# Kernel optimization log

Measured on AMD Instinct MI355X. Metric: run time of the kernel, lower is better.

Reference implementation:

```python
import jax, jax.numpy as jnp
import numpy as np

B, N, C = 4, 2048, 1024
H = 16
HD = C // H  # head_dim = 64


def setup_inputs() -> dict:
    key = jax.random.key(0)
    k1, k2, k3 = jax.random.split(key, 3)
    x = jax.random.normal(k1, (B, N, C), dtype=jnp.float32)
    # nn.Linear-style init scale ~ 1/sqrt(fan_in)
    W_qkv = jax.random.normal(k2, (3 * C, C), dtype=jnp.float32) / np.sqrt(C)
    W_proj = jax.random.normal(k3, (C, C), dtype=jnp.float32) / np.sqrt(C)
    b_proj = jnp.zeros((C,), dtype=jnp.float32)
    return {"x": x, "W_qkv": W_qkv, "W_proj": W_proj, "b_proj": b_proj}


def reference(x, W_qkv, W_proj, b_proj):
    Bb, Nn, Cc = x.shape
    scale = (Cc // H) ** -0.5
    # qkv: [B,N,3C] -> [3,B,H,N,HD]
    qkv = jnp.einsum('bnc,dc->bnd', x, W_qkv)
    qkv = qkv.reshape(Bb, Nn, 3, H, Cc // H).transpose(2, 0, 3, 1, 4)
    q, k, v = qkv[0] * scale, qkv[1], qkv[2]
    attn = jnp.einsum('bhqd,bhkd->bhqk', q, k)  # [B,H,N,N]
    attn = jax.nn.softmax(attn, axis=-1)
    out = jnp.einsum('bhqk,bhkd->bhqd', attn, v)  # [B,H,N,HD]
    out = out.transpose(0, 2, 1, 3).reshape(Bb, Nn, Cc)
    return jnp.einsum('bnc,dc->bnd', out, W_proj) + b_proj
```

## Files before the change

kernel.cpp:

```cpp
#include <hip/hip_runtime.h>

typedef _Float16 f16;
typedef _Float16 half8 __attribute__((ext_vector_type(8)));
typedef _Float16 half4 __attribute__((ext_vector_type(4)));
typedef __fp16 fp16x2 __attribute__((ext_vector_type(2)));
typedef float float4_ __attribute__((ext_vector_type(4)));
typedef float f32x16 __attribute__((ext_vector_type(16)));
typedef unsigned int uint2_ __attribute__((ext_vector_type(2)));

#define MFMA16(a, b, c) __builtin_amdgcn_mfma_f32_16x16x32_f16(a, b, c, 0, 0, 0)
#define MFMA32(a, b, c) __builtin_amdgcn_mfma_f32_32x32x16_f16(a, b, c, 0, 0, 0)

__device__ __forceinline__ void gld_lds16(const void* g, void* l) {
    __builtin_amdgcn_global_load_lds(
        (const __attribute__((address_space(1))) void*)g,
        (__attribute__((address_space(3))) void*)l, 16, 0, 0);
}

__device__ __forceinline__ unsigned pkrtz(float a, float b) {
    union { fp16x2 h; unsigned u; } c;
    c.h = __builtin_amdgcn_cvt_pkrtz(a, b);
    return c.u;
}

__device__ __forceinline__ float max3f(float a, float b, float c) {
    float d;
    asm("v_max3_f32 %0, %1, %2, %3" : "=v"(d) : "v"(a), "v"(b), "v"(c));
    return d;
}

__global__ void cast_kernel(const float* __restrict__ in, f16* __restrict__ out,
                            int n, int qboundary, float qscale) {
    int i = (blockIdx.x * blockDim.x + threadIdx.x) * 4;
    if (i >= n) return;
    float4_ v = *(const float4_*)(in + i);
    float sc = (i < qboundary) ? qscale : 1.0f;
    half4 h;
    h[0] = (f16)(v[0] * sc);
    h[1] = (f16)(v[1] * sc);
    h[2] = (f16)(v[2] * sc);
    h[3] = (f16)(v[3] * sc);
    *(half4*)(out + i) = h;
}

__global__ __launch_bounds__(256, 2)
void qkv_gemm(const f16* __restrict__ X, const f16* __restrict__ W,
              f16* __restrict__ Q, f16* __restrict__ Kq, f16* __restrict__ V) {
    const int K = 1024;
    __shared__ __align__(16) f16 sA[128 * 64];
    __shared__ __align__(16) f16 sB[128 * 64];
    int tid = threadIdx.x;
    int lane = tid & 63, wave = tid >> 6;
    int wm = wave >> 1, wn = wave & 1;
    int l15 = lane & 15, quad = lane >> 4;
    int rowBase = blockIdx.y * 128;
    int colBase = blockIdx.x * 128;

    float4_ acc[4][4] = {};

    for (int k0 = 0; k0 < K; k0 += 64) {
        for (int i = 0; i < 4; ++i) {
            int seg = wave * 4 + i;
            int e = (seg * 64 + lane) * 8;
            int r = e >> 6, c = e & 63;
            gld_lds16(X + (size_t)(rowBase + r) * K + k0 + c, sA + seg * 512);
            gld_lds16(W + (size_t)(colBase + r) * K + k0 + c, sB + seg * 512);
        }
        __syncthreads();
        for (int ks = 0; ks < 2; ++ks) {
            half8 a[4], b[4];
            for (int mt = 0; mt < 4; ++mt)
                a[mt] = *(const half8*)&sA[(wm * 64 + mt * 16 + l15) * 64 + ks * 32 + quad * 8];
            for (int nt = 0; nt < 4; ++nt)
                b[nt] = *(const half8*)&sB[(wn * 64 + nt * 16 + l15) * 64 + ks * 32 + quad * 8];
            for (int mt = 0; mt < 4; ++mt)
                for (int nt = 0; nt < 4; ++nt)
                    acc[mt][nt] = MFMA16(a[mt], b[nt], acc[mt][nt]);
        }
        __syncthreads();
    }

    for (int mt = 0; mt < 4; ++mt) {
        int m0 = rowBase + wm * 64 + mt * 16 + quad * 4;
        for (int nt = 0; nt < 4; ++nt) {
            int d = colBase + wn * 64 + nt * 16 + l15;
            int part = d >> 10;
            int h = (d >> 6) & 15;
            int hd = d & 63;
            f16* dst = (part == 0) ? Q : (part == 1) ? Kq : V;
            for (int r = 0; r < 4; ++r) {
                int m = m0 + r;
                int b = m >> 11, n = m & 2047;
                dst[(size_t)((b * 16 + h) * 2048 + n) * 64 + hd] = (f16)acc[mt][nt][r];
            }
        }
    }
}

__global__ __launch_bounds__(256, 2)
void attn_kernel(const f16* __restrict__ Q, const f16* __restrict__ Kk,
                 const f16* __restrict__ V, f16* __restrict__ O) {
    int L = blockIdx.y * gridDim.x + blockIdx.x;
    int m_ = L & 63;
    int bh = (m_ & 7) * 8 + (m_ >> 3);
    int qt = L >> 6;
    const f16* Qb = Q + (size_t)bh * 2048 * 64;
    const f16* Kb = Kk + (size_t)bh * 2048 * 64;
    const f16* Vb = V + (size_t)bh * 2048 * 64;
    int tid = threadIdx.x, lane = tid & 63, wave = tid >> 6;
    int l31 = lane & 31, hi = lane >> 5;

    __shared__ __align__(16) f16 Vt[2][64 * 72];

    int qbase = qt * 128 + wave * 32;

    half8 aQ[4];
#pragma unroll
    for (int d = 0; d < 4; ++d)
        aQ[d] = *(const half8*)(Qb + (size_t)(qbase + l31) * 64 + d * 16 + hi * 8);

    f32x16 oacc0 = {}, oacc1 = {}, lacc = {};
    float mrow = -1e30f;

    half8 vone;
#pragma unroll
    for (int j = 0; j < 8; ++j) vone[j] = (f16)1.0f;

    half8 bK0[4], bK1[4];
#pragma unroll
    for (int d = 0; d < 4; ++d) {
        bK0[d] = *(const half8*)(Kb + (size_t)(l31) * 64 + d * 16 + hi * 8);
        bK1[d] = *(const half8*)(Kb + (size_t)(32 + l31) * 64 + d * 16 + hi * 8);
    }
    {
        const f16* vsrc = Vb + (size_t)lane * 64 + wave * 16;
        half8 v0 = *(const half8*)(vsrc);
        half8 v1 = *(const half8*)(vsrc + 8);
#pragma unroll
        for (int j = 0; j < 8; ++j) {
            Vt[0][(wave * 16 + j) * 72 + lane] = v0[j];
            Vt[0][(wave * 16 + 8 + j) * 72 + lane] = v1[j];
        }
    }

#pragma unroll 2
    for (int it = 0; it < 32; ++it) {
        int buf = it & 1;
        __syncthreads();

        f32x16 s0 = {}, s1 = {};
        __builtin_amdgcn_s_setprio(1);
#pragma unroll
        for (int d = 0; d < 4; ++d) s0 = MFMA32(bK0[d], aQ[d], s0);
#pragma unroll
        for (int d = 0; d < 4; ++d) s1 = MFMA32(bK1[d], aQ[d], s1);
        __builtin_amdgcn_s_setprio(0);

        half8 bK0n[4], bK1n[4], v0n, v1n;
        if (it < 31) {
            int t1 = (it + 1) * 64;
#pragma unroll
            for (int d = 0; d < 4; ++d) {
                bK0n[d] = *(const half8*)(Kb + (size_t)(t1 + l31) * 64 + d * 16 + hi * 8);
                bK1n[d] = *(const half8*)(Kb + (size_t)(t1 + 32 + l31) * 64 + d * 16 + hi * 8);
            }
            const f16* vsrc = Vb + (size_t)(t1 + lane) * 64 + wave * 16;
            v0n = *(const half8*)(vsrc);
            v1n = *(const half8*)(vsrc + 8);
        }

        float a0 = max3f(s0[0], s0[1], s0[2]);
        float a1 = max3f(s0[3], s0[4], s0[5]);
        float a2 = max3f(s0[6], s0[7], s0[8]);
        float a3 = max3f(s0[9], s0[10], s0[11]);
        float a4 = max3f(s0[12], s0[13], s0[14]);
        float a5 = max3f(s0[15], s1[0], s1[1]);
        float a6 = max3f(s1[2], s1[3], s1[4]);
        float a7 = max3f(s1[5], s1[6], s1[7]);
        float a8 = max3f(s1[8], s1[9], s1[10]);
        float a9 = max3f(s1[11], s1[12], s1[13]);
        float a10 = fmaxf(s1[14], s1[15]);
        float b0 = max3f(a0, a1, a2);
        float b1 = max3f(a3, a4, a5);
        float b2 = max3f(a6, a7, a8);
        float b3 = fmaxf(a9, a10);
        float mx = fmaxf(max3f(b0, b1, b2), b3);
        mx = fmaxf(mx, __shfl_xor(mx, 32, 64));

        if (__any(mx > mrow + 8.0f)) {
            float mnew = fmaxf(mrow, mx);
            float alpha = exp2f(mrow - mnew);
            mrow = mnew;
#pragma unroll
            for (int r = 0; r < 16; ++r) {
                int cr = (r & 3) + 8 * (r >> 2) + 4 * hi;
                float ar = __shfl(alpha, cr, 64);
                oacc0[r] *= ar;
                oacc1[r] *= ar;
                lacc[r] *= ar;
            }
        }

#pragma unroll
        for (int r = 0; r < 16; ++r) s0[r] = exp2f(s0[r] - mrow);
#pragma unroll
        for (int r = 0; r < 16; ++r) s1[r] = exp2f(s1[r] - mrow);

        half8 PA[4];
        {
            union { half8 h; unsigned u[4]; } w;
            uint2_ r02 = __builtin_amdgcn_permlane32_swap(pkrtz(s0[0], s0[1]), pkrtz(s0[4], s0[5]), false, false);
            uint2_ r13 = __builtin_amdgcn_permlane32_swap(pkrtz(s0[2], s0[3]), pkrtz(s0[6], s0[7]), false, false);
            w.u[0] = r02[0]; w.u[1] = r13[0]; w.u[2] = r02[1]; w.u[3] = r13[1];
            PA[0] = w.h;
            r02 = __builtin_amdgcn_permlane32_swap(pkrtz(s0[8], s0[9]), pkrtz(s0[12], s0[13]), false, false);
            r13 = __builtin_amdgcn_permlane32_swap(pkrtz(s0[10], s0[11]), pkrtz(s0[14], s0[15]), false, false);
            w.u[0] = r02[0]; w.u[1] = r13[0]; w.u[2] = r02[1]; w.u[3] = r13[1];
            PA[1] = w.h;
            r02 = __builtin_amdgcn_permlane32_swap(pkrtz(s1[0], s1[1]), pkrtz(s1[4], s1[5]), false, false);
            r13 = __builtin_amdgcn_permlane32_swap(pkrtz(s1[2], s1[3]), pkrtz(s1[6], s1[7]), false, false);
            w.u[0] = r02[0]; w.u[1] = r13[0]; w.u[2] = r02[1]; w.u[3] = r13[1];
            PA[2] = w.h;
            r02 = __builtin_amdgcn_permlane32_swap(pkrtz(s1[8], s1[9]), pkrtz(s1[12], s1[13]), false, false);
            r13 = __builtin_amdgcn_permlane32_swap(pkrtz(s1[10], s1[11]), pkrtz(s1[14], s1[15]), false, false);
            w.u[0] = r02[0]; w.u[1] = r13[0]; w.u[2] = r02[1]; w.u[3] = r13[1];
            PA[3] = w.h;
        }

        __builtin_amdgcn_s_setprio(1);
#pragma unroll
        for (int ks = 0; ks < 4; ++ks) {
            half8 vf0 = *(const half8*)&Vt[buf][(l31) * 72 + ks * 16 + hi * 8];
            half8 vf1 = *(const half8*)&Vt[buf][(32 + l31) * 72 + ks * 16 + hi * 8];
            oacc0 = MFMA32(PA[ks], vf0, oacc0);
            oacc1 = MFMA32(PA[ks], vf1, oacc1);
            lacc = MFMA32(PA[ks], vone, lacc);
        }
        __builtin_amdgcn_s_setprio(0);

        if (it < 31) {
#pragma unroll
            for (int j = 0; j < 8; ++j) {
                Vt[buf ^ 1][(wave * 16 + j) * 72 + lane] = v0n[j];
                Vt[buf ^ 1][(wave * 16 + 8 + j) * 72 + lane] = v1n[j];
            }
#pragma unroll
            for (int d = 0; d < 4; ++d) {
                bK0[d] = bK0n[d];
                bK1[d] = bK1n[d];
            }
        }
    }

    int b = bh >> 4, h = bh & 15;
#pragma unroll
    for (int r = 0; r < 16; ++r) {
        int cr = (r & 3) + 8 * (r >> 2) + 4 * hi;
        int n = qbase + cr;
        float inv = 1.0f / lacc[r];
        O[(size_t)(b * 2048 + n) * 1024 + h * 64 + l31] = (f16)(oacc0[r] * inv);
        O[(size_t)(b * 2048 + n) * 1024 + h * 64 + 32 + l31] = (f16)(oacc1[r] * inv);
    }
}

__global__ __launch_bounds__(256, 2)
void proj_gemm(const f16* __restrict__ A, const f16* __restrict__ W,
               const float* __restrict__ bias, float* __restrict__ out) {
    const int K = 1024;
    __shared__ __align__(16) f16 sA[128 * 64];
    __shared__ __align__(16) f16 sB[128 * 64];
    int tid = threadIdx.x;
    int lane = tid & 63, wave = tid >> 6;
    int wm = wave >> 1, wn = wave & 1;
    int l15 = lane & 15, quad = lane >> 4;
    int rowBase = blockIdx.y * 128;
    int colBase = blockIdx.x * 128;

    float4_ acc[4][4] = {};

    for (int k0 = 0; k0 < K; k0 += 64) {
        for (int i = 0; i < 4; ++i) {
            int seg = wave * 4 + i;
            int e = (seg * 64 + lane) * 8;
            int r = e >> 6, c = e & 63;
            gld_lds16(A + (size_t)(rowBase + r) * K + k0 + c, sA + seg * 512);
            gld_lds16(W + (size_t)(colBase + r) * K + k0 + c, sB + seg * 512);
        }
        __syncthreads();
        for (int ks = 0; ks < 2; ++ks) {
            half8 a[4], b[4];
            for (int mt = 0; mt < 4; ++mt)
                a[mt] = *(const half8*)&sA[(wm * 64 + mt * 16 + l15) * 64 + ks * 32 + quad * 8];
            for (int nt = 0; nt < 4; ++nt)
                b[nt] = *(const half8*)&sB[(wn * 64 + nt * 16 + l15) * 64 + ks * 32 + quad * 8];
            for (int mt = 0; mt < 4; ++mt)
                for (int nt = 0; nt < 4; ++nt)
                    acc[mt][nt] = MFMA16(a[mt], b[nt], acc[mt][nt]);
        }
        __syncthreads();
    }

    for (int mt = 0; mt < 4; ++mt) {
        int m0 = rowBase + wm * 64 + mt * 16 + quad * 4;
        for (int nt = 0; nt < 4; ++nt) {
            int d = colBase + wn * 64 + nt * 16 + l15;
            float bv = bias[d];
            for (int r = 0; r < 4; ++r) {
                int m = m0 + r;
                out[(size_t)m * 1024 + d] = acc[mt][nt][r] + bv;
            }
        }
    }
}

extern "C" void kernel_launch(void* const* d_in, const int* in_sizes, int n_in,
                              void* d_out, int out_size, void* d_ws, size_t ws_size,
                              hipStream_t stream) {
    const float* x     = (const float*)d_in[0];
    const float* Wqkv  = (const float*)d_in[1];
    const float* Wproj = (const float*)d_in[2];
    const float* bproj = (const float*)d_in[3];
    float* out = (float*)d_out;

    f16* ws     = (f16*)d_ws;
    f16* xb     = ws;
    f16* wqkvb  = xb + 8388608;
    f16* wprojb = wqkvb + 3145728;
    f16* q      = wprojb + 1048576;
    f16* k      = q + 8388608;
    f16* v      = k + 8388608;
    f16* ao     = v + 8388608;

    const float qscale = 0.125f * 1.4426950408889634f;

    cast_kernel<<<8192, 256, 0, stream>>>(x, xb, 8388608, 0, 1.f);
    cast_kernel<<<3072, 256, 0, stream>>>(Wqkv, wqkvb, 3145728, 1048576, qscale);
    cast_kernel<<<1024, 256, 0, stream>>>(Wproj, wprojb, 1048576, 0, 1.f);

    qkv_gemm<<<dim3(24, 64), 256, 0, stream>>>(xb, wqkvb, q, k, v);
    attn_kernel<<<dim3(16, 64), 256, 0, stream>>>(q, k, v, ao);
    proj_gemm<<<dim3(8, 64), 256, 0, stream>>>(ao, wprojb, bproj, out);
}
```

Before: 344.4 us.

## Halve attention KV tile, compute row sums on VALU, merge cast kernels

Merges the three fp32-to-fp16 cast launches into one kernel that picks its source by index range. In the attention kernel the KV tile per iteration drops from 64 to 32 keys, giving more iterations with fewer live registers and a smaller LDS V buffer. K is prefetched one tile ahead and V two tiles ahead. The softmax denominator is now a VALU sum with a cross-half shuffle instead of an extra MFMA against a ones vector. The trade-off is more barriers and max/rescale checks per query block, in exchange for fewer MFMAs and lower register pressure.

```diff
diff --git a/kernel.cpp b/kernel.cpp
--- a/kernel.cpp
+++ b/kernel.cpp
@@ -29,12 +29,23 @@
     return d;
 }
 
-__global__ void cast_kernel(const float* __restrict__ in, f16* __restrict__ out,
-                            int n, int qboundary, float qscale) {
+__global__ void cast_all_kernel(const float* __restrict__ x,
+                                const float* __restrict__ wqkv,
+                                const float* __restrict__ wproj,
+                                f16* __restrict__ out, float qscale) {
     int i = (blockIdx.x * blockDim.x + threadIdx.x) * 4;
-    if (i >= n) return;
-    float4_ v = *(const float4_*)(in + i);
-    float sc = (i < qboundary) ? qscale : 1.0f;
+    const float* src;
+    float sc = 1.0f;
+    if (i < 8388608) {
+        src = x + i;
+    } else if (i < 11534336) {
+        int j = i - 8388608;
+        src = wqkv + j;
+        if (j < 1048576) sc = qscale;
+    } else {
+        src = wproj + (i - 11534336);
+    }
+    float4_ v = *(const float4_*)src;
     half4 h;
     h[0] = (f16)(v[0] * sc);
     h[1] = (f16)(v[1] * sc);
@@ -110,7 +121,7 @@
     int tid = threadIdx.x, lane = tid & 63, wave = tid >> 6;
     int l31 = lane & 31, hi = lane >> 5;
 
-    __shared__ __align__(16) f16 Vt[2][64 * 72];
+    __shared__ __align__(16) f16 Vt[2][64 * 40];
 
     int qbase = qt * 128 + wave * 32;
 
@@ -119,145 +130,111 @@
     for (int d = 0; d < 4; ++d)
         aQ[d] = *(const half8*)(Qb + (size_t)(qbase + l31) * 64 + d * 16 + hi * 8);
 
-    f32x16 oacc0 = {}, oacc1 = {}, lacc = {};
-    float mrow = -1e30f;
-
-    half8 vone;
-#pragma unroll
-    for (int j = 0; j < 8; ++j) vone[j] = (f16)1.0f;
-
-    half8 bK0[4], bK1[4];
-#pragma unroll
-    for (int d = 0; d < 4; ++d) {
-        bK0[d] = *(const half8*)(Kb + (size_t)(l31) * 64 + d * 16 + hi * 8);
-        bK1[d] = *(const half8*)(Kb + (size_t)(32 + l31) * 64 + d * 16 + hi * 8);
-    }
-    {
-        const f16* vsrc = Vb + (size_t)lane * 64 + wave * 16;
-        half8 v0 = *(const half8*)(vsrc);
-        half8 v1 = *(const half8*)(vsrc + 8);
-#pragma unroll
-        for (int j = 0; j < 8; ++j) {
-            Vt[0][(wave * 16 + j) * 72 + lane] = v0[j];
-            Vt[0][(wave * 16 + 8 + j) * 72 + lane] = v1[j];
-        }
-    }
+    f32x16 oacc0 = {}, oacc1 = {};
+    float lsum = 0.f, mrow = -1e30f;
+
+    half8 vreg = *(const half8*)(Vb + (size_t)(l31) * 64 + wave * 16 + hi * 8);
+#pragma unroll
+    for (int j = 0; j < 8; ++j)
+        Vt[0][(wave * 16 + hi * 8 + j) * 40 + l31] = vreg[j];
+    vreg = *(const half8*)(Vb + (size_t)(32 + l31) * 64 + wave * 16 + hi * 8);
+    half8 bK[4];
+#pragma unroll
+    for (int d = 0; d < 4; ++d)
+        bK[d] = *(const half8*)(Kb + (size_t)(l31) * 64 + d * 16 + hi * 8);
 
 #pragma unroll 2
-    for (int it = 0; it < 32; ++it) {
+    for (int it = 0; it < 64; ++it) {
         int buf = it & 1;
         __syncthreads();
 
-        f32x16 s0 = {}, s1 = {};
+        f32x16 s = {};
         __builtin_amdgcn_s_setprio(1);
 #pragma unroll
-        for (int d = 0; d < 4; ++d) s0 = MFMA32(bK0[d], aQ[d], s0);
-#pragma unroll
-        for (int d = 0; d < 4; ++d) s1 = MFMA32(bK1[d], aQ[d], s1);
+        for (int d = 0; d < 4; ++d) s = MFMA32(bK[d], aQ[d], s);
         __builtin_amdgcn_s_setprio(0);
 
-        half8 bK0n[4], bK1n[4], v0n, v1n;
-        if (it < 31) {
-            int t1 = (it + 1) * 64;
-#pragma unroll
-            for (int d = 0; d < 4; ++d) {
-                bK0n[d] = *(const half8*)(Kb + (size_t)(t1 + l31) * 64 + d * 16 + hi * 8);
-                bK1n[d] = *(const half8*)(Kb + (size_t)(t1 + 32 + l31) * 64 + d * 16 + hi * 8);
-            }
-            const f16* vsrc = Vb + (size_t)(t1 + lane) * 64 + wave * 16;
-            v0n = *(const half8*)(vsrc);
-            v1n = *(const half8*)(vsrc + 8);
-        }
-
-        float a0 = max3f(s0[0], s0[1], s0[2]);
-        float a1 = max3f(s0[3], s0[4], s0[5]);
-        float a2 = max3f(s0[6], s0[7], s0[8]);
-        float a3 = max3f(s0[9], s0[10], s0[11]);
-        float a4 = max3f(s0[12], s0[13], s0[14]);
-        float a5 = max3f(s0[15], s1[0], s1[1]);
-        float a6 = max3f(s1[2], s1[3], s1[4]);
-        float a7 = max3f(s1[5], s1[6], s1[7]);
-        float a8 = max3f(s1[8], s1[9], s1[10]);
-        float a9 = max3f(s1[11], s1[12], s1[13]);
-        float a10 = fmaxf(s1[14], s1[15]);
+        {
+            int kt = (it + 1 < 64) ? it + 1 : 63;
+#pragma unroll
+            for (int d = 0; d < 4; ++d)
+                bK[d] = *(const half8*)(Kb + (size_t)(kt * 32 + l31) * 64 + d * 16 + hi * 8);
+        }
+#pragma unroll
+        for (int j = 0; j < 8; ++j)
+            Vt[buf ^ 1][(wave * 16 + hi * 8 + j) * 40 + l31] = vreg[j];
+        {
+            int vt = (it + 2 < 64) ? it + 2 : 63;
+            vreg = *(const half8*)(Vb + (size_t)(vt * 32 + l31) * 64 + wave * 16 + hi * 8);
+        }
+
+        float a0 = max3f(s[0], s[1], s[2]);
+        float a1 = max3f(s[3], s[4], s[5]);
+        float a2 = max3f(s[6], s[7], s[8]);
+        float a3 = max3f(s[9], s[10], s[11]);
+        float a4 = max3f(s[12], s[13], s[14]);
         float b0 = max3f(a0, a1, a2);
-        float b1 = max3f(a3, a4, a5);
-        float b2 = max3f(a6, a7, a8);
-        float b3 = fmaxf(a9, a10);
-        float mx = fmaxf(max3f(b0, b1, b2), b3);
+        float b1 = max3f(a3, a4, s[15]);
+        float mx = fmaxf(b0, b1);
         mx = fmaxf(mx, __shfl_xor(mx, 32, 64));
 
         if (__any(mx > mrow + 8.0f)) {
             float mnew = fmaxf(mrow, mx);
             float alpha = exp2f(mrow - mnew);
             mrow = mnew;
+            lsum *= alpha;
 #pragma unroll
             for (int r = 0; r < 16; ++r) {
                 int cr = (r & 3) + 8 * (r >> 2) + 4 * hi;
                 float ar = __shfl(alpha, cr, 64);
                 oacc0[r] *= ar;
                 oacc1[r] *= ar;
-                lacc[r] *= ar;
             }
         }
 
 #pragma unroll
-        for (int r = 0; r < 16; ++r) s0[r] = exp2f(s0[r] - mrow);
-#pragma unroll
-        for (int r = 0; r < 16; ++r) s1[r] = exp2f(s1[r] - mrow);
-
-        half8 PA[4];
+        for (int r = 0; r < 16; ++r) s[r] = exp2f(s[r] - mrow);
+        {
+            float t0 = (s[0] + s[1]) + (s[2] + s[3]);
+            float t1 = (s[4] + s[5]) + (s[6] + s[7]);
+            float t2 = (s[8] + s[9]) + (s[10] + s[11]);
+            float t3 = (s[12] + s[13]) + (s[14] + s[15]);
+            float ts = (t0 + t1) + (t2 + t3);
+            ts += __shfl_xor(ts, 32, 64);
+            lsum += ts;
+        }
+
+        half8 PA[2];
         {
             union { half8 h; unsigned u[4]; } w;
-            uint2_ r02 = __builtin_amdgcn_permlane32_swap(pkrtz(s0[0], s0[1]), pkrtz(s0[4], s0[5]), false, false);
-            uint2_ r13 = __builtin_amdgcn_permlane32_swap(pkrtz(s0[2], s0[3]), pkrtz(s0[6], s0[7]), false, false);
+            uint2_ r02 = __builtin_amdgcn_permlane32_swap(pkrtz(s[0], s[1]), pkrtz(s[4], s[5]), false, false);
+            uint2_ r13 = __builtin_amdgcn_permlane32_swap(pkrtz(s[2], s[3]), pkrtz(s[6], s[7]), false, false);
             w.u[0] = r02[0]; w.u[1] = r13[0]; w.u[2] = r02[1]; w.u[3] = r13[1];
             PA[0] = w.h;
-            r02 = __builtin_amdgcn_permlane32_swap(pkrtz(s0[8], s0[9]), pkrtz(s0[12], s0[13]), false, false);
-            r13 = __builtin_amdgcn_permlane32_swap(pkrtz(s0[10], s0[11]), pkrtz(s0[14], s0[15]), false, false);
+            r02 = __builtin_amdgcn_permlane32_swap(pkrtz(s[8], s[9]), pkrtz(s[12], s[13]), false, false);
+            r13 = __builtin_amdgcn_permlane32_swap(pkrtz(s[10], s[11]), pkrtz(s[14], s[15]), false, false);
             w.u[0] = r02[0]; w.u[1] = r13[0]; w.u[2] = r02[1]; w.u[3] = r13[1];
             PA[1] = w.h;
-            r02 = __builtin_amdgcn_permlane32_swap(pkrtz(s1[0], s1[1]), pkrtz(s1[4], s1[5]), false, false);
-            r13 = __builtin_amdgcn_permlane32_swap(pkrtz(s1[2], s1[3]), pkrtz(s1[6], s1[7]), false, false);
-            w.u[0] = r02[0]; w.u[1] = r13[0]; w.u[2] = r02[1]; w.u[3] = r13[1];
-            PA[2] = w.h;
-            r02 = __builtin_amdgcn_permlane32_swap(pkrtz(s1[8], s1[9]), pkrtz(s1[12], s1[13]), false, false);
-            r13 = __builtin_amdgcn_permlane32_swap(pkrtz(s1[10], s1[11]), pkrtz(s1[14], s1[15]), false, false);
-            w.u[0] = r02[0]; w.u[1] = r13[0]; w.u[2] = r02[1]; w.u[3] = r13[1];
-            PA[3] = w.h;
         }
 
         __builtin_amdgcn_s_setprio(1);
 #pragma unroll
-        for (int ks = 0; ks < 4; ++ks) {
-            half8 vf0 = *(const half8*)&Vt[buf][(l31) * 72 + ks * 16 + hi * 8];
-            half8 vf1 = *(const half8*)&Vt[buf][(32 + l31) * 72 + ks * 16 + hi * 8];
+        for (int ks = 0; ks < 2; ++ks) {
+            half8 vf0 = *(const half8*)&Vt[buf][(l31) * 40 + ks * 16 + hi * 8];
+            half8 vf1 = *(const half8*)&Vt[buf][(32 + l31) * 40 + ks * 16 + hi * 8];
             oacc0 = MFMA32(PA[ks], vf0, oacc0);
             oacc1 = MFMA32(PA[ks], vf1, oacc1);
-            lacc = MFMA32(PA[ks], vone, lacc);
         }
         __builtin_amdgcn_s_setprio(0);
-
-        if (it < 31) {
-#pragma unroll
-            for (int j = 0; j < 8; ++j) {
-                Vt[buf ^ 1][(wave * 16 + j) * 72 + lane] = v0n[j];
-                Vt[buf ^ 1][(wave * 16 + 8 + j) * 72 + lane] = v1n[j];
-            }
-#pragma unroll
-            for (int d = 0; d < 4; ++d) {
-                bK0[d] = bK0n[d];
-                bK1[d] = bK1n[d];
-            }
-        }
     }
 
     int b = bh >> 4, h = bh & 15;
+    float invl = 1.0f / lsum;
 #pragma unroll
     for (int r = 0; r < 16; ++r) {
         int cr = (r & 3) + 8 * (r >> 2) + 4 * hi;
         int n = qbase + cr;
-        float inv = 1.0f / lacc[r];
+        float inv = __shfl(invl, cr, 64);
         O[(size_t)(b * 2048 + n) * 1024 + h * 64 + l31] = (f16)(oacc0[r] * inv);
         O[(size_t)(b * 2048 + n) * 1024 + h * 64 + 32 + l31] = (f16)(oacc1[r] * inv);
     }
@@ -333,9 +310,7 @@
 
     const float qscale = 0.125f * 1.4426950408889634f;
 
-    cast_kernel<<<8192, 256, 0, stream>>>(x, xb, 8388608, 0, 1.f);
-    cast_kernel<<<3072, 256, 0, stream>>>(Wqkv, wqkvb, 3145728, 1048576, qscale);
-    cast_kernel<<<1024, 256, 0, stream>>>(Wproj, wprojb, 1048576, 0, 1.f);
+    cast_all_kernel<<<12288, 256, 0, stream>>>(x, Wqkv, Wproj, ws, qscale);
 
     qkv_gemm<<<dim3(24, 64), 256, 0, stream>>>(xb, wqkvb, q, k, v);
     attn_kernel<<<dim3(16, 64), 256, 0, stream>>>(q, k, v, ao);
```

Result: no change. 338.1 us (-1.8%).
